# Optimization experiments

Hardware: AMD Instinct MI355X
Metric: run time of the kernel (lower is better)

## Reference

```python
import jax, jax.numpy as jnp
import numpy as np

H = 768
B = 65536
T = 3
EPS = 1e-5


def setup_inputs() -> dict:
    key = jax.random.key(0)
    ks = jax.random.split(key, 6)
    s = 1.0 / np.sqrt(H)
    return {
        "features": jax.random.normal(ks[0], (B, T, H), dtype=jnp.float32),
        "Wq": jax.random.normal(ks[1], (H, H), dtype=jnp.float32) * s,
        "bq": jnp.zeros((H,), jnp.float32),
        "Wk": jax.random.normal(ks[2], (H, H), dtype=jnp.float32) * s,
        "bk": jnp.zeros((H,), jnp.float32),
        "Wv": jax.random.normal(ks[3], (H, H), dtype=jnp.float32) * s,
        "bv": jnp.zeros((H,), jnp.float32),
        "Wo": jax.random.normal(ks[4], (H, H), dtype=jnp.float32) * s,
        "bo": jnp.zeros((H,), jnp.float32),
        "ln_g": jnp.ones((H,), jnp.float32),
        "ln_b": jnp.zeros((H,), jnp.float32),
    }


def reference(features, Wq, bq, Wk, bk, Wv, bv, Wo, bo, ln_g, ln_b):
    # LayerNorm over last dim
    mu = jnp.mean(features, axis=-1, keepdims=True)
    var = jnp.mean(jnp.square(features - mu), axis=-1, keepdims=True)
    x = (features - mu) * jax.lax.rsqrt(var + EPS) * ln_g + ln_b  # [B,T,H]

    scale = H ** (-0.5)
    Q = jnp.einsum("bth,oh->bto", x, Wq) + bq
    K = jnp.einsum("bth,oh->bto", x, Wk) + bk
    V = jnp.einsum("bth,oh->bto", x, Wv) + bv

    Qp, Qn = jax.nn.relu(Q), jax.nn.relu(-Q)
    Kp, Kn = jax.nn.relu(K), jax.nn.relu(-K)

    attn_pos = jax.nn.softmax(jnp.einsum("bqh,bkh->bqk", Qp, Kp) * scale, axis=-1)
    attn_neg = jax.nn.softmax(jnp.einsum("bqh,bkh->bqk", Qn, Kn) * scale, axis=-1)

    out = jnp.einsum("bqk,bkh->bqh", attn_pos, V) - jnp.einsum("bqk,bkh->bqh", attn_neg, V)
    out = jnp.einsum("bth,oh->bto", out, Wo) + bo
    return x + out
```

## Files before the change

kernel.cpp:

```cpp
#include <hip/hip_runtime.h>

typedef __attribute__((ext_vector_type(8))) _Float16 half8;
typedef __attribute__((ext_vector_type(4))) _Float16 half4;
typedef __attribute__((ext_vector_type(4))) float f32x4;

#define HDIM 768
#define LNEPS 1e-5f

#define L_AS   0
#define L_BS   24576
#define L_STQ  57344
#define L_STK  108032
#define L_SP   158720
#define L_SN   161024
#define L_TOT  163328
#define SSTR   264

__device__ __forceinline__ void gload_lds16(const void* g, void* l) {
  __builtin_amdgcn_global_load_lds(
      (const __attribute__((address_space(1))) void*)g,
      (__attribute__((address_space(3))) void*)l, 16, 0, 0);
}

__global__ __launch_bounds__(256) void convert_kernel(
    const float* __restrict__ Wq, const float* __restrict__ Wk,
    const float* __restrict__ bq, const float* __restrict__ bk,
    _Float16* __restrict__ Wf, float* __restrict__ biasf)
{
  const long NW = 1536L * 768;
  long i = (long)blockIdx.x * 256 + threadIdx.x;
  if (i < NW) {
    const int orow = (int)(i / 768);
    const int k = (int)(i - (long)orow * 768);
    const int n = orow >> 8, c = orow & 255;
    const int src = n * 128 + (c & 127);
    Wf[i] = (_Float16)((c < 128) ? Wq[(long)src * 768 + k]
                                 : Wk[(long)src * 768 + k]);
  } else if (i < NW + 1536) {
    const int j = (int)(i - NW);
    const int n = j >> 8, c = j & 255;
    const int src = n * 128 + (c & 127);
    biasf[j] = (c < 128) ? bq[src] : bk[src];
  }
}

__global__ __launch_bounds__(256) void wvo_kernel(
    const float* __restrict__ Wo, const float* __restrict__ Wv,
    const float* __restrict__ bv,
    _Float16* __restrict__ Wvo, float* __restrict__ bvo)
{
  if (blockIdx.x == 144) {
    for (int o = threadIdx.x; o < 768; o += 256) {
      float s = 0.f;
      for (int h = 0; h < 768; ++h) s += Wo[o * 768 + h] * bv[h];
      bvo[o] = s;
    }
    return;
  }
  __shared__ float As[64][65];
  __shared__ float Bs[64][65];
  const int bm = blockIdx.x / 12, bn = blockIdx.x % 12;
  const int tid = threadIdx.x;
  const int tr = tid >> 4, tc = tid & 15;
  float acc[4][4] = {};
  for (int k0 = 0; k0 < 768; k0 += 64) {
    __syncthreads();
#pragma unroll
    for (int i = 0; i < 16; ++i) {
      const int e = i * 256 + tid, r = e >> 6, c = e & 63;
      As[r][c] = Wo[(bm * 64 + r) * 768 + (k0 + c)];
      Bs[r][c] = Wv[(k0 + r) * 768 + (bn * 64 + c)];
    }
    __syncthreads();
#pragma unroll 8
    for (int k = 0; k < 64; ++k) {
      float a[4], b[4];
#pragma unroll
      for (int i = 0; i < 4; ++i) a[i] = As[tr * 4 + i][k];
#pragma unroll
      for (int j = 0; j < 4; ++j) b[j] = Bs[k][tc * 4 + j];
#pragma unroll
      for (int i = 0; i < 4; ++i)
#pragma unroll
        for (int j = 0; j < 4; ++j) acc[i][j] += a[i] * b[j];
    }
  }
#pragma unroll
  for (int i = 0; i < 4; ++i)
#pragma unroll
    for (int j = 0; j < 4; ++j)
      Wvo[(bm * 64 + tr * 4 + i) * 768 + bn * 64 + tc * 4 + j] = (_Float16)acc[i][j];
}

__global__ __launch_bounds__(256) void ln_kernel(
    const float* __restrict__ feat, const float* __restrict__ gamma,
    const float* __restrict__ beta, _Float16* __restrict__ xout)
{
  const int w = threadIdx.x >> 6, lane = threadIdx.x & 63;
  const long row = (long)blockIdx.x * 4 + w;
  const float* fr = feat + row * HDIM;
  float4 v[3];
  float s = 0.f, ss = 0.f;
#pragma unroll
  for (int i = 0; i < 3; ++i) {
    v[i] = *(const float4*)&fr[(i * 64 + lane) * 4];
    s  += v[i].x + v[i].y + v[i].z + v[i].w;
    ss += v[i].x * v[i].x + v[i].y * v[i].y + v[i].z * v[i].z + v[i].w * v[i].w;
  }
#pragma unroll
  for (int off = 32; off; off >>= 1) {
    s  += __shfl_xor(s, off);
    ss += __shfl_xor(ss, off);
  }
  const float mu = s * (1.f / 768.f);
  const float var = ss * (1.f / 768.f) - mu * mu;
  const float rs = rsqrtf(var + LNEPS);
#pragma unroll
  for (int i = 0; i < 3; ++i) {
    const int idx = (i * 64 + lane) * 4;
    float4 g4 = *(const float4*)&gamma[idx];
    float4 b4 = *(const float4*)&beta[idx];
    half4 o;
    o[0] = (_Float16)((v[i].x - mu) * rs * g4.x + b4.x);
    o[1] = (_Float16)((v[i].y - mu) * rs * g4.y + b4.y);
    o[2] = (_Float16)((v[i].z - mu) * rs * g4.z + b4.z);
    o[3] = (_Float16)((v[i].w - mu) * rs * g4.w + b4.w);
    *(half4*)&xout[row * HDIM + idx] = o;
  }
}

__global__ __launch_bounds__(512, 1) void fused_kernel(
    const _Float16* __restrict__ xh,
    const _Float16* __restrict__ Wf,
    const float* __restrict__ bias,
    const float* __restrict__ bo,
    float* __restrict__ out)
{
  __shared__ __align__(16) char lds[L_TOT];
  const int tid = threadIdx.x;
  const int lane = tid & 63;
  const int quad = lane >> 4, l16 = lane & 15;
  const int w = tid >> 6;
  const int wm = w >> 2, wn = w & 3;

  const int nwg = gridDim.x;
  const int orig = blockIdx.x;
  const int bid = (orig & 7) * (nwg >> 3) + (orig >> 3);
  const long m0 = (long)bid * 192;

  {
    float* sc = (float*)(lds + L_SP);
#pragma unroll
    for (int i = 0; i < 3; ++i) {
      const int idx = i * 512 + tid;
      if (idx < 1152) sc[idx] = 0.f;
    }
  }

  const int wg = w & 3;
  long aOff[3]; int aLds[3];
#pragma unroll
  for (int i = 0; i < 3; ++i) {
    const int c = i * 256 + wg * 64 + lane, r = c >> 2, p = c & 3;
    const int cc = p ^ ((r >> 1) & 3);
    aOff[i] = (m0 + r) * HDIM + cc * 8;
    aLds[i] = c * 16;
  }
  long bOff[4]; int bLds[4];
#pragma unroll
  for (int i = 0; i < 4; ++i) {
    const int c = i * 256 + wg * 64 + lane, r = c >> 2, p = c & 3;
    const int cc = p ^ ((r >> 1) & 3);
    bOff[i] = (long)r * HDIM + cc * 8;
    bLds[i] = c * 16;
  }

  int stg_buf = 0; long stg_k = 0; long stg_nb = 0;
#define STAGE()                                                               \
  do {                                                                        \
    if (w < 4) {                                                              \
      _Pragma("unroll")                                                       \
      for (int i_ = 0; i_ < 3; ++i_)                                          \
        gload_lds16(xh + aOff[i_] + stg_k, lds + L_AS + stg_buf * 12288 + aLds[i_]); \
    } else {                                                                  \
      _Pragma("unroll")                                                       \
      for (int i_ = 0; i_ < 4; ++i_)                                          \
        gload_lds16(Wf + stg_nb + bOff[i_] + stg_k, lds + L_BS + stg_buf * 16384 + bLds[i_]); \
    }                                                                         \
    stg_buf ^= 1; stg_k += 32;                                                \
    if (stg_k == HDIM) { stg_k = 0; stg_nb += 256L * HDIM; }                  \
  } while (0)

#define FRAGREAD(AF_, BF_, buf_)                                              \
  do {                                                                        \
    const char* as_ = lds + L_AS + (buf_) * 12288;                            \
    const char* bs_ = lds + L_BS + (buf_) * 16384;                            \
    _Pragma("unroll")                                                         \
    for (int mi_ = 0; mi_ < 6; ++mi_) {                                       \
      const int r_ = wm * 96 + mi_ * 16 + l16;                                \
      AF_[mi_] = *(const half8*)(as_ + r_ * 64 + ((quad ^ ((r_ >> 1) & 3)) * 16)); \
    }                                                                         \
    _Pragma("unroll")                                                         \
    for (int ni_ = 0; ni_ < 4; ++ni_) {                                       \
      const int r_ = wn * 64 + ni_ * 16 + l16;                                \
      BF_[ni_] = *(const half8*)(bs_ + r_ * 64 + ((quad ^ ((r_ >> 1) & 3)) * 16)); \
    }                                                                         \
  } while (0)

#define STEPBODY(s_, CURA_, CURB_, NXTA_, NXTB_, nbuf_)                       \
  do {                                                                        \
    asm volatile("s_waitcnt lgkmcnt(0)" ::: "memory");                        \
    __builtin_amdgcn_sched_barrier(0);                                        \
    asm volatile("s_waitcnt vmcnt(0)" ::: "memory");                          \
    __builtin_amdgcn_sched_barrier(0);                                        \
    __builtin_amdgcn_s_barrier();         \
    __builtin_amdgcn_sched_barrier(0);                                        \
    if ((s_) < 214) STAGE();                      \
    if ((s_) < 215) FRAGREAD(NXTA_, NXTB_, (nbuf_));                          \
    __builtin_amdgcn_s_setprio(1);                                            \
    _Pragma("unroll")                                                         \
    for (int mi_ = 0; mi_ < 6; ++mi_)                                         \
      _Pragma("unroll")                                                       \
      for (int ni_ = 0; ni_ < 4; ++ni_)                                       \
        acc[mi_][ni_] = __builtin_amdgcn_mfma_f32_16x16x32_f16(               \
            CURA_[mi_], CURB_[ni_], acc[mi_][ni_], 0, 0, 0);                  \
    __builtin_amdgcn_s_setprio(0);                                            \
    __builtin_amdgcn_sched_barrier(0);                                        \
  } while (0)

  f32x4 acc[6][4];
#pragma unroll
  for (int mi = 0; mi < 6; ++mi)
#pragma unroll
    for (int ni = 0; ni < 4; ++ni)
#pragma unroll
      for (int j = 0; j < 4; ++j) acc[mi][ni][j] = 0.f;

  half8 afA[6], bfA[4], afB[6], bfB[4];

  STAGE();
  asm volatile("s_waitcnt vmcnt(0)" ::: "memory");
  __builtin_amdgcn_sched_barrier(0);
  __builtin_amdgcn_s_barrier();
  __builtin_amdgcn_sched_barrier(0);
  FRAGREAD(afA, bfA, 0);
  STAGE();

  for (int n = 0; n < 9; ++n) {
    for (int ks2 = 0; ks2 < 12; ++ks2) {
      const int s0 = n * 24 + ks2 * 2;
      STEPBODY(s0, afA, bfA, afB, bfB, 1);
      const int s1 = s0 + 1;
      STEPBODY(s1, afB, bfB, afA, bfA, 0);
    }

    {
      float bv[4];
#pragma unroll
      for (int ni = 0; ni < 4; ++ni)
        bv[ni] = bias[n * 256 + wn * 64 + ni * 16 + l16];
      char* st = lds + ((wn >> 1) ? L_STK : L_STQ);
      const int cb = (wn & 1) * 64;
#pragma unroll
      for (int mi = 0; mi < 6; ++mi)
#pragma unroll
        for (int ni = 0; ni < 4; ++ni)
#pragma unroll
          for (int j = 0; j < 4; ++j) {
            const int row = wm * 96 + mi * 16 + quad * 4 + j;
            *(_Float16*)(st + row * SSTR + (cb + ni * 16 + l16) * 2) =
                (_Float16)(acc[mi][ni][j] + bv[ni]);
          }
#pragma unroll
      for (int mi = 0; mi < 6; ++mi)
#pragma unroll
        for (int ni = 0; ni < 4; ++ni)
#pragma unroll
          for (int j = 0; j < 4; ++j) acc[mi][ni][j] = 0.f;
    }
    __builtin_amdgcn_s_barrier();

    if (n < 6) {
      const int b = tid >> 3, sub = tid & 7;
      half4 qv[3][4], kv[3][4];
#pragma unroll
      for (int t = 0; t < 3; ++t) {
        const char* rq = lds + L_STQ + (3 * b + t) * SSTR + sub * 32;
        const char* rk = lds + L_STK + (3 * b + t) * SSTR + sub * 32;
#pragma unroll
        for (int u = 0; u < 4; ++u) {
          qv[t][u] = *(const half4*)(rq + u * 8);
          kv[t][u] = *(const half4*)(rk + u * 8);
        }
      }
#pragma unroll
      for (int qi = 0; qi < 3; ++qi)
#pragma unroll
        for (int ki = 0; ki < 3; ++ki) {
          float p = 0.f, nn = 0.f;
#pragma unroll
          for (int u = 0; u < 4; ++u)
#pragma unroll
            for (int e = 0; e < 4; ++e) {
              const float qq = (float)qv[qi][u][e];
              const float kk = (float)kv[ki][u][e];
              p  += fmaxf(qq, 0.f) * fmaxf(kk, 0.f);
              nn += fminf(qq, 0.f) * fminf(kk, 0.f);
            }
          p  += __shfl_xor(p, 1);  p  += __shfl_xor(p, 2);  p  += __shfl_xor(p, 4);
          nn += __shfl_xor(nn, 1); nn += __shfl_xor(nn, 2); nn += __shfl_xor(nn, 4);
          if (sub == 0) {
            ((float*)(lds + L_SP))[b * 9 + qi * 3 + ki] += p;
            ((float*)(lds + L_SN))[b * 9 + qi * 3 + ki] += nn;
          }
        }
      __builtin_amdgcn_s_barrier();
      if (n == 5) {
        if (tid < 64) {
          float* sp = (float*)(lds + L_SP) + tid * 9;
          float* sn = (float*)(lds + L_SN) + tid * 9;
          const float scale = 0.03608439182435161f;
#pragma unroll
          for (int qi = 0; qi < 3; ++qi) {
            const float p0 = sp[qi*3+0]*scale, p1 = sp[qi*3+1]*scale, p2 = sp[qi*3+2]*scale;
            const float n0 = sn[qi*3+0]*scale, n1 = sn[qi*3+1]*scale, n2 = sn[qi*3+2]*scale;
            const float mp = fmaxf(p0, fmaxf(p1, p2));
            const float mn = fmaxf(n0, fmaxf(n1, n2));
            const float ep0 = __expf(p0-mp), ep1 = __expf(p1-mp), ep2 = __expf(p2-mp);
            const float en0 = __expf(n0-mn), en1 = __expf(n1-mn), en2 = __expf(n2-mn);
            const float rp = 1.f / (ep0+ep1+ep2), rn = 1.f / (en0+en1+en2);
            sp[qi*3+0] = ep0*rp - en0*rn;
            sp[qi*3+1] = ep1*rp - en1*rn;
            sp[qi*3+2] = ep2*rp - en2*rn;
          }
        }
        __builtin_amdgcn_s_barrier();
      }
    } else {
      const int cg = tid & 63, rg = tid >> 6;
      const int c = cg * 4;
      const char* vb = lds + ((c >> 7) ? L_STK : L_STQ) + (c & 127) * 2;
      const long gc = 256L * (n - 6) + c;
      const f32x4 bov = *(const f32x4*)&bo[gc];
      const float* cf0 = (const float*)(lds + L_SP);
#pragma unroll 4
      for (int rr = 0; rr < 24; ++rr) {
        const int row = rr * 8 + rg;
        const int b = (int)((unsigned)row / 3u);
        const int t = row - 3 * b;
        const float* cf = cf0 + b * 9 + t * 3;
        const half4 v0 = *(const half4*)(vb + (3 * b + 0) * SSTR);
        const half4 v1 = *(const half4*)(vb + (3 * b + 1) * SSTR);
        const half4 v2 = *(const half4*)(vb + (3 * b + 2) * SSTR);
        const half4 hx = *(const half4*)&xh[(m0 + row) * HDIM + gc];
        const float c0 = cf[0], c1 = cf[1], c2 = cf[2];
        f32x4 o;
#pragma unroll
        for (int j = 0; j < 4; ++j)
          o[j] = (float)hx[j] + bov[j] + c0 * (float)v0[j]
               + c1 * (float)v1[j] + c2 * (float)v2[j];
        *(f32x4*)&out[(m0 + row) * HDIM + gc] = o;
      }
      __builtin_amdgcn_s_barrier();
    }
  }
#undef STAGE
#undef FRAGREAD
#undef STEPBODY
}

extern "C" void kernel_launch(void* const* d_in, const int* in_sizes, int n_in,
                              void* d_out, int out_size, void* d_ws, size_t ws_size,
                              hipStream_t stream) {
  (void)in_sizes; (void)n_in; (void)out_size; (void)ws_size;
  const float* feat = (const float*)d_in[0];
  const float* Wq   = (const float*)d_in[1];
  const float* bq   = (const float*)d_in[2];
  const float* Wk   = (const float*)d_in[3];
  const float* bk   = (const float*)d_in[4];
  const float* Wv   = (const float*)d_in[5];
  const float* bv   = (const float*)d_in[6];
  const float* Wo   = (const float*)d_in[7];
  const float* bo   = (const float*)d_in[8];
  const float* ln_g = (const float*)d_in[9];
  const float* ln_b = (const float*)d_in[10];

  char* ws = (char*)d_ws;
  _Float16* xh    = (_Float16*)(ws);
  _Float16* Wf    = (_Float16*)(ws + 301989888L);
  float*    biasf = (float*)   (ws + 305528832L);

  convert_kernel<<<4614, 256, 0, stream>>>(Wq, Wk, bq, bk, Wf, biasf);
  wvo_kernel<<<145, 256, 0, stream>>>(Wo, Wv, bv, Wf + 1536L * 768, biasf + 1536);
  ln_kernel<<<49152, 256, 0, stream>>>(feat, ln_g, ln_b, xh);
  fused_kernel<<<1024, 512, 0, stream>>>(xh, Wf, biasf, bo, (float*)d_out);
}
```

Baseline: 1.320 ms.

## Use four-slot LDS ring aliased onto staging buffers with partial vmcnt waits

Replaces the two-slot double buffer, which waited for all loads and hit a barrier every k-step, with a four-slot ring of A/B tiles. The slots alias the Q/K staging regions, which cuts the LDS footprint and may allow higher occupancy. Two k-slices are staged per half-iteration and vmcnt waits only for the older group, so loads run further ahead of the MFMAs. The cost is two barriers per half-iteration and the whole pipeline restarting per n-block. There is also a risk of overwriting staging data through the aliased LDS region.

After: 1.526 ms. 15.6% more time.

```diff
diff --git a/kernel.cpp b/kernel.cpp
--- a/kernel.cpp
+++ b/kernel.cpp
@@ -7,14 +7,15 @@
 #define HDIM 768
 #define LNEPS 1e-5f
 
-#define L_AS   0
-#define L_BS   24576
-#define L_STQ  57344
-#define L_STK  108032
-#define L_SP   158720
-#define L_SN   161024
-#define L_TOT  163328
+#define L_STQ  0
+#define L_STK  57344
+#define L_SP   114688
+#define L_SN   116992
+#define L_TOT  119296
 #define SSTR   264
+
+#define A_BASE(q_) ((((q_) & 2) ? 57344 : 0) + ((q_) & 1) * 12288)
+#define B_BASE(q_) ((((q_) & 2) ? 57344 : 0) + 24576 + ((q_) & 1) * 16384)
 
 __device__ __forceinline__ void gload_lds16(const void* g, void* l) {
   __builtin_amdgcn_global_load_lds(
@@ -175,26 +176,27 @@
     bLds[i] = c * 16;
   }
 
-  int stg_buf = 0; long stg_k = 0; long stg_nb = 0;
-#define STAGE()                                                               \
+#define STAGEH(q_, h_)                                                        \
   do {                                                                        \
+    const long hk_ = (long)(h_) * 32;                                         \
     if (w < 4) {                                                              \
       _Pragma("unroll")                                                       \
       for (int i_ = 0; i_ < 3; ++i_)                                          \
-        gload_lds16(xh + aOff[i_] + stg_k, lds + L_AS + stg_buf * 12288 + aLds[i_]); \
+        gload_lds16(xh + aOff[i_] + hk_, lds + A_BASE(q_) + aLds[i_]);        \
     } else {                                                                  \
       _Pragma("unroll")                                                       \
       for (int i_ = 0; i_ < 4; ++i_)                                          \
-        gload_lds16(Wf + stg_nb + bOff[i_] + stg_k, lds + L_BS + stg_buf * 16384 + bLds[i_]); \
+        gload_lds16(Wf + bNb + bOff[i_] + hk_, lds + B_BASE(q_) + bLds[i_]);  \
     }                                                                         \
-    stg_buf ^= 1; stg_k += 32;                                                \
-    if (stg_k == HDIM) { stg_k = 0; stg_nb += 256L * HDIM; }                  \
   } while (0)
-
-#define FRAGREAD(AF_, BF_, buf_)                                              \
+#define VMW()                                                                 \
+  do { if (w < 4) { asm volatile("s_waitcnt vmcnt(6)" ::: "memory"); }        \
+       else       { asm volatile("s_waitcnt vmcnt(8)" ::: "memory"); } } while (0)
+
+#define FRAGREAD(AF_, BF_, q_)                                                \
   do {                                                                        \
-    const char* as_ = lds + L_AS + (buf_) * 12288;                            \
-    const char* bs_ = lds + L_BS + (buf_) * 16384;                            \
+    const char* as_ = lds + A_BASE(q_);                                       \
+    const char* bs_ = lds + B_BASE(q_);                                       \
     _Pragma("unroll")                                                         \
     for (int mi_ = 0; mi_ < 6; ++mi_) {                                       \
       const int r_ = wm * 96 + mi_ * 16 + l16;                                \
@@ -207,27 +209,18 @@
     }                                                                         \
   } while (0)
 
-#define STEPBODY(s_, CURA_, CURB_, NXTA_, NXTB_, nbuf_)                       \
+#define MFMA24(AF_, BF_)                                                      \
   do {                                                                        \
-    asm volatile("s_waitcnt lgkmcnt(0)" ::: "memory");                        \
-    __builtin_amdgcn_sched_barrier(0);                                        \
-    asm volatile("s_waitcnt vmcnt(0)" ::: "memory");                          \
-    __builtin_amdgcn_sched_barrier(0);                                        \
-    __builtin_amdgcn_s_barrier();         \
-    __builtin_amdgcn_sched_barrier(0);                                        \
-    if ((s_) < 214) STAGE();                      \
-    if ((s_) < 215) FRAGREAD(NXTA_, NXTB_, (nbuf_));                          \
-    __builtin_amdgcn_s_setprio(1);                                            \
     _Pragma("unroll")                                                         \
     for (int mi_ = 0; mi_ < 6; ++mi_)                                         \
       _Pragma("unroll")                                                       \
       for (int ni_ = 0; ni_ < 4; ++ni_)                                       \
         acc[mi_][ni_] = __builtin_amdgcn_mfma_f32_16x16x32_f16(               \
-            CURA_[mi_], CURB_[ni_], acc[mi_][ni_], 0, 0, 0);                  \
-    __builtin_amdgcn_s_setprio(0);                                            \
-    __builtin_amdgcn_sched_barrier(0);                                        \
+            AF_[mi_], BF_[ni_], acc[mi_][ni_], 0, 0, 0);                      \
   } while (0)
 
+#define SB0() __builtin_amdgcn_sched_barrier(0)
+
   f32x4 acc[6][4];
 #pragma unroll
   for (int mi = 0; mi < 6; ++mi)
@@ -236,22 +229,45 @@
 #pragma unroll
       for (int j = 0; j < 4; ++j) acc[mi][ni][j] = 0.f;
 
-  half8 afA[6], bfA[4], afB[6], bfB[4];
-
-  STAGE();
-  asm volatile("s_waitcnt vmcnt(0)" ::: "memory");
-  __builtin_amdgcn_sched_barrier(0);
-  __builtin_amdgcn_s_barrier();
-  __builtin_amdgcn_sched_barrier(0);
-  FRAGREAD(afA, bfA, 0);
-  STAGE();
+  half8 af0[6], bf0[4], af1[6], bf1[4];
 
   for (int n = 0; n < 9; ++n) {
-    for (int ks2 = 0; ks2 < 12; ++ks2) {
-      const int s0 = n * 24 + ks2 * 2;
-      STEPBODY(s0, afA, bfA, afB, bfB, 1);
-      const int s1 = s0 + 1;
-      STEPBODY(s1, afB, bfB, afA, bfA, 0);
+    const long bNb = (long)n * (256L * HDIM);
+
+    STAGEH(0, 0); STAGEH(1, 1); STAGEH(2, 2); STAGEH(3, 3);
+    VMW();
+    SB0();
+    __builtin_amdgcn_s_barrier();
+    SB0();
+
+    for (int i = 0; i < 6; ++i) {
+      FRAGREAD(af0, bf0, 0);
+      FRAGREAD(af1, bf1, 1);
+      __builtin_amdgcn_s_setprio(1);
+      MFMA24(af0, bf0);
+      MFMA24(af1, bf1);
+      __builtin_amdgcn_s_setprio(0);
+      SB0();
+      __builtin_amdgcn_s_barrier();
+      SB0();
+      if (i < 5) { STAGEH(0, 4 * i + 4); STAGEH(1, 4 * i + 5); VMW(); }
+      else       { asm volatile("s_waitcnt vmcnt(0)" ::: "memory"); }
+      SB0();
+      __builtin_amdgcn_s_barrier();
+      SB0();
+      FRAGREAD(af0, bf0, 2);
+      FRAGREAD(af1, bf1, 3);
+      __builtin_amdgcn_s_setprio(1);
+      MFMA24(af0, bf0);
+      MFMA24(af1, bf1);
+      __builtin_amdgcn_s_setprio(0);
+      SB0();
+      __builtin_amdgcn_s_barrier();
+      SB0();
+      if (i < 5) { STAGEH(2, 4 * i + 6); STAGEH(3, 4 * i + 7); VMW(); }
+      SB0();
+      __builtin_amdgcn_s_barrier();
+      SB0();
     }
 
     {
@@ -364,9 +380,11 @@
       __builtin_amdgcn_s_barrier();
     }
   }
-#undef STAGE
+#undef STAGEH
+#undef VMW
 #undef FRAGREAD
-#undef STEPBODY
+#undef MFMA24
+#undef SB0
 }
 
 extern "C" void kernel_launch(void* const* d_in, const int* in_sizes, int n_in,
```

## Restructure QKV GEMM main loop to keep one global tile load in flight

Applied to the files above, without the earlier changes.

The main loop drops the register double-buffered fragment prefetch. Each step now reads LDS fragments, runs the MFMAs, barriers, then issues the global-to-LDS load two steps ahead and waits with a partial vmcnt, so one tile load stays outstanding instead of draining vmcnt(0) every step. This is meant to hide global load latency better and free the registers of the second fragment set. The cost is a second barrier per step and LDS fragment reads that are no longer overlapped with the previous step's MFMAs.

Measured after the change: 1.234 ms, median of 3. -6.6%, faster.

```diff
diff --git a/kernel.cpp b/kernel.cpp
--- a/kernel.cpp
+++ b/kernel.cpp
@@ -175,83 +175,82 @@
     bLds[i] = c * 16;
   }
 
-  int stg_buf = 0; long stg_k = 0; long stg_nb = 0;
-#define STAGE()                                                               \
+  long stg_k = 0, stg_nb = 0;
+#define STAGE(BUF_)                                                           \
   do {                                                                        \
     if (w < 4) {                                                              \
       _Pragma("unroll")                                                       \
       for (int i_ = 0; i_ < 3; ++i_)                                          \
-        gload_lds16(xh + aOff[i_] + stg_k, lds + L_AS + stg_buf * 12288 + aLds[i_]); \
+        gload_lds16(xh + aOff[i_] + stg_k, lds + L_AS + (BUF_) * 12288 + aLds[i_]); \
     } else {                                                                  \
       _Pragma("unroll")                                                       \
       for (int i_ = 0; i_ < 4; ++i_)                                          \
-        gload_lds16(Wf + stg_nb + bOff[i_] + stg_k, lds + L_BS + stg_buf * 16384 + bLds[i_]); \
+        gload_lds16(Wf + stg_nb + bOff[i_] + stg_k, lds + L_BS + (BUF_) * 16384 + bLds[i_]); \
     }                                                                         \
-    stg_buf ^= 1; stg_k += 32;                                                \
+    stg_k += 32;                                                              \
     if (stg_k == HDIM) { stg_k = 0; stg_nb += 256L * HDIM; }                  \
   } while (0)
-
-#define FRAGREAD(AF_, BF_, buf_)                                              \
+#define VMW()                                                                 \
+  do { if (w < 4) { asm volatile("s_waitcnt vmcnt(3)" ::: "memory"); }        \
+       else       { asm volatile("s_waitcnt vmcnt(4)" ::: "memory"); } } while (0)
+#define SB0() __builtin_amdgcn_sched_barrier(0)
+
+  f32x4 acc[6][4];
+#pragma unroll
+  for (int mi = 0; mi < 6; ++mi)
+#pragma unroll
+    for (int ni = 0; ni < 4; ++ni)
+#pragma unroll
+      for (int j = 0; j < 4; ++j) acc[mi][ni][j] = 0.f;
+
+#define STEPK(BUF_, s_)                                                       \
   do {                                                                        \
-    const char* as_ = lds + L_AS + (buf_) * 12288;                            \
-    const char* bs_ = lds + L_BS + (buf_) * 16384;                            \
+    const char* as_ = lds + L_AS + (BUF_) * 12288;                            \
+    const char* bs_ = lds + L_BS + (BUF_) * 16384;                            \
+    half8 af[6], bf[4];                                                       \
     _Pragma("unroll")                                                         \
     for (int mi_ = 0; mi_ < 6; ++mi_) {                                       \
       const int r_ = wm * 96 + mi_ * 16 + l16;                                \
-      AF_[mi_] = *(const half8*)(as_ + r_ * 64 + ((quad ^ ((r_ >> 1) & 3)) * 16)); \
+      af[mi_] = *(const half8*)(as_ + r_ * 64 + ((quad ^ ((r_ >> 1) & 3)) * 16)); \
     }                                                                         \
     _Pragma("unroll")                                                         \
     for (int ni_ = 0; ni_ < 4; ++ni_) {                                       \
       const int r_ = wn * 64 + ni_ * 16 + l16;                                \
-      BF_[ni_] = *(const half8*)(bs_ + r_ * 64 + ((quad ^ ((r_ >> 1) & 3)) * 16)); \
+      bf[ni_] = *(const half8*)(bs_ + r_ * 64 + ((quad ^ ((r_ >> 1) & 3)) * 16)); \
     }                                                                         \
-  } while (0)
-
-#define STEPBODY(s_, CURA_, CURB_, NXTA_, NXTB_, nbuf_)                       \
-  do {                                                                        \
-    asm volatile("s_waitcnt lgkmcnt(0)" ::: "memory");                        \
-    __builtin_amdgcn_sched_barrier(0);                                        \
-    asm volatile("s_waitcnt vmcnt(0)" ::: "memory");                          \
-    __builtin_amdgcn_sched_barrier(0);                                        \
-    __builtin_amdgcn_s_barrier();         \
-    __builtin_amdgcn_sched_barrier(0);                                        \
-    if ((s_) < 214) STAGE();                      \
-    if ((s_) < 215) FRAGREAD(NXTA_, NXTB_, (nbuf_));                          \
     __builtin_amdgcn_s_setprio(1);                                            \
     _Pragma("unroll")                                                         \
     for (int mi_ = 0; mi_ < 6; ++mi_)                                         \
       _Pragma("unroll")                                                       \
       for (int ni_ = 0; ni_ < 4; ++ni_)                                       \
         acc[mi_][ni_] = __builtin_amdgcn_mfma_f32_16x16x32_f16(               \
-            CURA_[mi_], CURB_[ni_], acc[mi_][ni_], 0, 0, 0);                  \
+            af[mi_], bf[ni_], acc[mi_][ni_], 0, 0, 0);                        \
     __builtin_amdgcn_s_setprio(0);                                            \
-    __builtin_amdgcn_sched_barrier(0);                                        \
+    SB0();                                                                    \
+    __builtin_amdgcn_s_barrier();             \
+    SB0();                                                                    \
+    if ((s_) + 2 < 216) STAGE(BUF_);         \
+    if ((s_) < 214) {                                                         \
+      VMW();                                             \
+      __builtin_amdgcn_s_barrier();                                           \
+      SB0();                                                                  \
+    } else if ((s_) == 214) {                                                 \
+      asm volatile("s_waitcnt vmcnt(0)" ::: "memory");              \
+      __builtin_amdgcn_s_barrier();                                           \
+      SB0();                                                                  \
+    }                                                                         \
   } while (0)
 
-  f32x4 acc[6][4];
-#pragma unroll
-  for (int mi = 0; mi < 6; ++mi)
-#pragma unroll
-    for (int ni = 0; ni < 4; ++ni)
-#pragma unroll
-      for (int j = 0; j < 4; ++j) acc[mi][ni][j] = 0.f;
-
-  half8 afA[6], bfA[4], afB[6], bfB[4];
-
-  STAGE();
-  asm volatile("s_waitcnt vmcnt(0)" ::: "memory");
-  __builtin_amdgcn_sched_barrier(0);
+  STAGE(0); STAGE(1);
+  VMW();
   __builtin_amdgcn_s_barrier();
-  __builtin_amdgcn_sched_barrier(0);
-  FRAGREAD(afA, bfA, 0);
-  STAGE();
+  SB0();
 
   for (int n = 0; n < 9; ++n) {
     for (int ks2 = 0; ks2 < 12; ++ks2) {
-      const int s0 = n * 24 + ks2 * 2;
-      STEPBODY(s0, afA, bfA, afB, bfB, 1);
-      const int s1 = s0 + 1;
-      STEPBODY(s1, afB, bfB, afA, bfA, 0);
+      const int sbase = n * 24 + ks2 * 2;
+      STEPK(0, sbase);
+      STEPK(1, sbase + 1);
     }
 
     {
@@ -365,8 +364,9 @@
     }
   }
 #undef STAGE
-#undef FRAGREAD
-#undef STEPBODY
+#undef VMW
+#undef SB0
+#undef STEPK
 }
 
 extern "C" void kernel_launch(void* const* d_in, const int* in_sizes, int n_in,
```
